# Performance work log

Hardware: AMD Instinct MI355X
Metric: run time of the kernel (lower is better)

## Reference

```python
import jax, jax.numpy as jnp
import numpy as np

N = 100000      # nodes
E = 1600000     # edges
F_IN = 64       # num_features
H = 64          # nhid
G = 512         # num graphs in batch
C = 2           # num_classes
BN_EPS = 1e-5


def setup_inputs() -> dict:
    key = jax.random.key(0)
    ks = jax.random.split(key, 8)
    x = jax.random.normal(ks[0], (N, F_IN), jnp.float32)
    edge_index = jax.random.randint(ks[1], (2, E), 0, N, dtype=jnp.int64)
    batch = jnp.sort(jax.random.randint(ks[2], (N,), 0, G, dtype=jnp.int64))
    s = lambda k, shp, fan: (jax.random.normal(k, shp, jnp.float32) / np.sqrt(fan)).astype(jnp.float32)
    W1 = s(ks[3], (F_IN, H), F_IN); b1 = jnp.zeros((H,), jnp.float32)
    W2 = s(ks[4], (H, H), H);       b2 = jnp.zeros((H,), jnp.float32)
    Wg = s(ks[5], (H, 1), H);       bg = jnp.zeros((1,), jnp.float32)
    bn_gamma = jnp.ones((H,), jnp.float32); bn_beta = jnp.zeros((H,), jnp.float32)
    bn_mean = jnp.zeros((H,), jnp.float32); bn_var = jnp.ones((H,), jnp.float32)
    W_lin = s(ks[6], (H, C), H);    b_lin = jnp.zeros((C,), jnp.float32)
    return dict(x=x, edge_index=edge_index, batch=batch,
                W1=W1, b1=b1, W2=W2, b2=b2, Wg=Wg, bg=bg,
                bn_gamma=bn_gamma, bn_beta=bn_beta, bn_mean=bn_mean, bn_var=bn_var,
                W_lin=W_lin, b_lin=b_lin)


def reference(x, edge_index, batch, W1, b1, W2, b2, Wg, bg,
              bn_gamma, bn_beta, bn_mean, bn_var, W_lin, b_lin):
    src, dst = edge_index[0], edge_index[1]
    # GINConv (eps=0): h_i = MLP(x_i + sum_{j->i} x_j)
    agg = jax.ops.segment_sum(x[src], dst, num_segments=N)       # [N, F_IN]
    h = x + agg
    h = jnp.maximum(h @ W1 + b1, 0.0) @ W2 + b2                  # [N, H]
    h = jnp.maximum(h, 0.0)                                      # outer ReLU
    # Attentional aggregation: segment softmax of gate, weighted segment-sum
    gate = (h @ Wg + bg)[:, 0]                                   # [N]
    gmax = jax.ops.segment_max(gate, batch, num_segments=G)      # [G]
    ex = jnp.exp(gate - gmax[batch])                             # [N]
    denom = jax.ops.segment_sum(ex, batch, num_segments=G)       # [G]
    alpha = ex / denom[batch]                                    # [N]
    pooled = jax.ops.segment_sum(alpha[:, None] * h, batch, num_segments=G)  # [G, H]
    # BatchNorm1d in eval mode (running stats); dropout is identity in eval
    norm = (pooled - bn_mean) / jnp.sqrt(bn_var + BN_EPS) * bn_gamma + bn_beta
    logits = norm @ W_lin + b_lin                                # [G, C]
    return jax.nn.log_softmax(logits, axis=-1)
```

## Files before the change

kernel.cpp:

```cpp
#include <hip/hip_runtime.h>
#include <math.h>
#include <float.h>

#define BN_EPS 1e-5f
#define PBLK   8192
#define NBUCKP 832
#define ACAP   4096
#define STCAP  3072

typedef short s16x8 __attribute__((ext_vector_type(8)));
typedef float f32x4 __attribute__((ext_vector_type(4)));

__device__ __forceinline__ unsigned short f2bf(float f) {
    unsigned u = __float_as_uint(f);
    u += 0x7FFFu + ((u >> 16) & 1u);
    return (unsigned short)(u >> 16);
}
__device__ __forceinline__ float bf2f(unsigned short b) {
    return __uint_as_float(((unsigned)b) << 16);
}
__device__ __forceinline__ int vtb(int row, int byteoff) {
    return row * 128 + (byteoff ^ ((row & 7) << 4));
}

__global__ __launch_bounds__(512) void prep_partition(
    const float* __restrict__ W1, const float* __restrict__ W2,
    unsigned short* __restrict__ w1t, unsigned short* __restrict__ w2t,
    const int* __restrict__ src, const int* __restrict__ dst,
    const int* __restrict__ batch, int* __restrict__ gstart,
    int* __restrict__ bcur0, int* __restrict__ packed2,
    int N, int E, int EB, int G)
{
    __shared__ int hist[NBUCKP], lstart[NBUCKP], goff[NBUCKP], cur[NBUCKP];
    __shared__ int sorted[PBLK];
    __shared__ unsigned short sbkt[PBLK];

    int tid = threadIdx.x;
    int lane = tid & 63;
    int blk = blockIdx.x;

    for (int i = blk * 512 + tid; i < N; i += gridDim.x * 512) {
        int bi = batch[i];
        int bp = (i == 0) ? -1 : batch[i - 1];
        for (int g = bp + 1; g <= bi; ++g) gstart[g] = i;
        if (i == N - 1)
            for (int g = bi + 1; g <= G; ++g) gstart[g] = N;
    }
    if (blk == 0)
        for (int idx = tid; idx < 4096; idx += 512)
            w1t[idx] = f2bf(W1[(idx & 63) * 64 + (idx >> 6)]);
    if (blk == 1)
        for (int idx = tid; idx < 4096; idx += 512)
            w2t[idx] = f2bf(W2[(idx & 63) * 64 + (idx >> 6)]);

    if (blk >= EB) return;

    int e0 = blk * PBLK;
    int cnt = E - e0; if (cnt > PBLK) cnt = PBLK; if (cnt < 0) cnt = 0;

    for (int i = tid; i < NBUCKP; i += 512) hist[i] = 0;
    __syncthreads();
    for (int i = tid; i < cnt; i += 512)
        atomicAdd(&hist[dst[e0 + i] >> 7], 1);
    __syncthreads();
    if (tid < 64) {
        int carry = 0;
        #pragma unroll
        for (int c = 0; c < NBUCKP / 64; ++c) {
            int idx = c * 64 + lane;
            int v = hist[idx];
            int xv = v;
            #pragma unroll
            for (int d = 1; d < 64; d <<= 1) {
                int t = __shfl_up(xv, d); if (lane >= d) xv += t;
            }
            lstart[idx] = xv - v + carry;
            carry += __shfl(xv, 63);
        }
    }
    __syncthreads();
    for (int i = tid; i < NBUCKP; i += 512) {
        cur[i] = lstart[i];
        if (hist[i] > 0) goff[i] = atomicAdd(&bcur0[i], hist[i]);
    }
    __syncthreads();
    for (int i = tid; i < cnt; i += 512) {
        int d = dst[e0 + i];
        int s = src[e0 + i];
        int b = d >> 7;
        int p = atomicAdd(&cur[b], 1);
        sorted[p] = ((d & 127) << 17) | s;
        sbkt[p] = (unsigned short)b;
    }
    __syncthreads();
    for (int i = tid; i < cnt; i += 512) {
        int b = sbkt[i];
        packed2[(size_t)b * ACAP + goff[b] + (i - lstart[b])] = sorted[i];
    }
}

__global__ __launch_bounds__(512, 4) void bucket_fused(
    const float* __restrict__ x,
    const int* __restrict__ packed2, const int* __restrict__ bcur0,
    const unsigned short* __restrict__ w1t, const unsigned short* __restrict__ w2t,
    const float* __restrict__ b1, const float* __restrict__ b2,
    const float* __restrict__ Wg, const float* __restrict__ bg,
    unsigned short* __restrict__ h_out, float* __restrict__ gate_out, int N)
{
    __shared__ char vt_raw[16384];
    __shared__ int stage[STCAP];
    int* hist = (int*)vt_raw;
    int* cur  = hist + 128;
    int* excl = (int*)(vt_raw + 1024);

    int tid = threadIdx.x;
    int lane = tid & 63;
    int wave = tid >> 6;
    int b = blockIdx.x;
    int node0 = b * 128;
    int ecnt = bcur0[b];
    if (ecnt > ACAP) ecnt = ACAP;
    const int* arena = packed2 + (size_t)b * ACAP;

    if (tid < 128) hist[tid] = 0;
    __syncthreads();
    for (int i = tid; i < ecnt; i += 512)
        atomicAdd(&hist[arena[i] >> 17], 1);
    __syncthreads();

    if (tid < 64) {
        int carry = 0;
        #pragma unroll
        for (int c = 0; c < 2; ++c) {
            int idx = c * 64 + lane;
            int v = hist[idx];
            int xv = v;
            #pragma unroll
            for (int d = 1; d < 64; d <<= 1) {
                int t = __shfl_up(xv, d); if (lane >= d) xv += t;
            }
            excl[idx] = xv - v + carry;
            cur[idx]  = xv - v + carry;
            carry += __shfl(xv, 63);
        }
        if (lane == 0) excl[128] = carry;
    }
    __syncthreads();

    for (int i = tid; i < ecnt; i += 512) {
        int v = arena[i];
        int p = atomicAdd(&cur[v >> 17], 1);
        if (p < STCAP) stage[p] = v & 0x1FFFF;
    }
    __syncthreads();

    int rowbase = wave * 16;
    int exv = excl[rowbase + (lane < 17 ? lane : 16)];
    if (exv > STCAP) exv = STCAP;
    __syncthreads();

    for (int m = 0; m < 16; ++m) {
        int ln = rowbase + m;
        int node = node0 + ln;
        if (node < N) {
            int beg  = __builtin_amdgcn_readlane(exv, m);
            int end_ = __builtin_amdgcn_readlane(exv, m + 1);

            float v0 = x[(unsigned)node * 64u + lane];
            float v1 = 0.f, v2 = 0.f, v3 = 0.f, v4 = 0.f, v5 = 0.f, v6 = 0.f, v7 = 0.f;

            for (int base = beg; base < end_; base += 64) {
                int eiv = (base + lane < end_) ? stage[base + lane] : 0;
                int cnt = end_ - base; if (cnt > 64) cnt = 64;
                int j = 0;
                for (; j + 16 <= cnt; j += 16) {
                    int s0  = __builtin_amdgcn_readlane(eiv, j + 0);
                    int s1  = __builtin_amdgcn_readlane(eiv, j + 1);
                    int s2  = __builtin_amdgcn_readlane(eiv, j + 2);
                    int s3  = __builtin_amdgcn_readlane(eiv, j + 3);
                    int s4  = __builtin_amdgcn_readlane(eiv, j + 4);
                    int s5  = __builtin_amdgcn_readlane(eiv, j + 5);
                    int s6  = __builtin_amdgcn_readlane(eiv, j + 6);
                    int s7  = __builtin_amdgcn_readlane(eiv, j + 7);
                    int s8  = __builtin_amdgcn_readlane(eiv, j + 8);
                    int s9  = __builtin_amdgcn_readlane(eiv, j + 9);
                    int s10 = __builtin_amdgcn_readlane(eiv, j + 10);
                    int s11 = __builtin_amdgcn_readlane(eiv, j + 11);
                    int s12 = __builtin_amdgcn_readlane(eiv, j + 12);
                    int s13 = __builtin_amdgcn_readlane(eiv, j + 13);
                    int s14 = __builtin_amdgcn_readlane(eiv, j + 14);
                    int s15 = __builtin_amdgcn_readlane(eiv, j + 15);
                    float t0  = x[(unsigned)s0  * 64u + lane];
                    float t1  = x[(unsigned)s1  * 64u + lane];
                    float t2  = x[(unsigned)s2  * 64u + lane];
                    float t3  = x[(unsigned)s3  * 64u + lane];
                    float t4  = x[(unsigned)s4  * 64u + lane];
                    float t5  = x[(unsigned)s5  * 64u + lane];
                    float t6  = x[(unsigned)s6  * 64u + lane];
                    float t7  = x[(unsigned)s7  * 64u + lane];
                    float t8  = x[(unsigned)s8  * 64u + lane];
                    float t9  = x[(unsigned)s9  * 64u + lane];
                    float t10 = x[(unsigned)s10 * 64u + lane];
                    float t11 = x[(unsigned)s11 * 64u + lane];
                    float t12 = x[(unsigned)s12 * 64u + lane];
                    float t13 = x[(unsigned)s13 * 64u + lane];
                    float t14 = x[(unsigned)s14 * 64u + lane];
                    float t15 = x[(unsigned)s15 * 64u + lane];
                    v0 += t0; v1 += t1; v2 += t2; v3 += t3;
                    v4 += t4; v5 += t5; v6 += t6; v7 += t7;
                    v0 += t8; v1 += t9; v2 += t10; v3 += t11;
                    v4 += t12; v5 += t13; v6 += t14; v7 += t15;
                }
                for (; j + 8 <= cnt; j += 8) {
                    int s0 = __builtin_amdgcn_readlane(eiv, j + 0);
                    int s1 = __builtin_amdgcn_readlane(eiv, j + 1);
                    int s2 = __builtin_amdgcn_readlane(eiv, j + 2);
                    int s3 = __builtin_amdgcn_readlane(eiv, j + 3);
                    int s4 = __builtin_amdgcn_readlane(eiv, j + 4);
                    int s5 = __builtin_amdgcn_readlane(eiv, j + 5);
                    int s6 = __builtin_amdgcn_readlane(eiv, j + 6);
                    int s7 = __builtin_amdgcn_readlane(eiv, j + 7);
                    float t0 = x[(unsigned)s0 * 64u + lane];
                    float t1 = x[(unsigned)s1 * 64u + lane];
                    float t2 = x[(unsigned)s2 * 64u + lane];
                    float t3 = x[(unsigned)s3 * 64u + lane];
                    float t4 = x[(unsigned)s4 * 64u + lane];
                    float t5 = x[(unsigned)s5 * 64u + lane];
                    float t6 = x[(unsigned)s6 * 64u + lane];
                    float t7 = x[(unsigned)s7 * 64u + lane];
                    v0 += t0; v1 += t1; v2 += t2; v3 += t3;
                    v4 += t4; v5 += t5; v6 += t6; v7 += t7;
                }
                for (; j + 4 <= cnt; j += 4) {
                    int s0 = __builtin_amdgcn_readlane(eiv, j + 0);
                    int s1 = __builtin_amdgcn_readlane(eiv, j + 1);
                    int s2 = __builtin_amdgcn_readlane(eiv, j + 2);
                    int s3 = __builtin_amdgcn_readlane(eiv, j + 3);
                    float t0 = x[(unsigned)s0 * 64u + lane];
                    float t1 = x[(unsigned)s1 * 64u + lane];
                    float t2 = x[(unsigned)s2 * 64u + lane];
                    float t3 = x[(unsigned)s3 * 64u + lane];
                    v4 += t0; v5 += t1; v6 += t2; v7 += t3;
                }
                for (; j < cnt; ++j) {
                    int s = __builtin_amdgcn_readlane(eiv, j);
                    v1 += x[(unsigned)s * 64u + lane];
                }
            }
            float v = ((v0 + v1) + (v2 + v3)) + ((v4 + v5) + (v6 + v7));
            *(unsigned short*)(vt_raw + vtb(ln, lane * 2)) = f2bf(v);
        } else {
            *(unsigned short*)(vt_raw + vtb(ln, lane * 2)) = 0;
        }
    }

    {
        int quad = lane >> 4;
        int col  = lane & 15;

        s16x8 a0 = *(const s16x8*)(vt_raw + vtb(rowbase + col, quad * 16));
        s16x8 a1 = *(const s16x8*)(vt_raw + vtb(rowbase + col, 64 + quad * 16));

        float b1v[4], b2v[4], wgv[4];
        #pragma unroll
        for (int nt = 0; nt < 4; ++nt) {
            b1v[nt] = b1[nt * 16 + col];
            b2v[nt] = b2[nt * 16 + col];
            wgv[nt] = Wg[nt * 16 + col];
        }
        float bgv = bg[0];

        f32x4 acc1[4];
        #pragma unroll
        for (int nt = 0; nt < 4; ++nt) {
            int off = (nt * 16 + col) * 64 + quad * 8;
            s16x8 w0 = *(const s16x8*)(w1t + off);
            s16x8 w1 = *(const s16x8*)(w1t + off + 32);
            f32x4 c = {0.f, 0.f, 0.f, 0.f};
            c = __builtin_amdgcn_mfma_f32_16x16x32_bf16(a0, w0, c, 0, 0, 0);
            c = __builtin_amdgcn_mfma_f32_16x16x32_bf16(a1, w1, c, 0, 0, 0);
            acc1[nt] = c;
        }
        #pragma unroll
        for (int nt = 0; nt < 4; ++nt)
            #pragma unroll
            for (int r = 0; r < 4; ++r) {
                float hv = fmaxf(acc1[nt][r] + b1v[nt], 0.f);
                *(unsigned short*)(vt_raw + vtb(rowbase + quad * 4 + r, (nt * 16 + col) * 2)) = f2bf(hv);
            }

        s16x8 g0 = *(const s16x8*)(vt_raw + vtb(rowbase + col, quad * 16));
        s16x8 g1 = *(const s16x8*)(vt_raw + vtb(rowbase + col, 64 + quad * 16));

        f32x4 acc2[4];
        #pragma unroll
        for (int nt = 0; nt < 4; ++nt) {
            int off = (nt * 16 + col) * 64 + quad * 8;
            s16x8 w0 = *(const s16x8*)(w2t + off);
            s16x8 w1 = *(const s16x8*)(w2t + off + 32);
            f32x4 c = {0.f, 0.f, 0.f, 0.f};
            c = __builtin_amdgcn_mfma_f32_16x16x32_bf16(g0, w0, c, 0, 0, 0);
            c = __builtin_amdgcn_mfma_f32_16x16x32_bf16(g1, w1, c, 0, 0, 0);
            acc2[nt] = c;
        }

        int nbase = node0 + rowbase;
        float gp[4] = {0.f, 0.f, 0.f, 0.f};
        #pragma unroll
        for (int nt = 0; nt < 4; ++nt)
            #pragma unroll
            for (int r = 0; r < 4; ++r) {
                float hv = fmaxf(acc2[nt][r] + b2v[nt], 0.f);
                int node = nbase + quad * 4 + r;
                if (node < N)
                    h_out[(size_t)node * 64 + nt * 16 + col] = f2bf(hv);
                gp[r] = fmaf(hv, wgv[nt], gp[r]);
            }
        #pragma unroll
        for (int r = 0; r < 4; ++r) {
            float t = gp[r];
            t += __shfl_xor(t, 1);
            t += __shfl_xor(t, 2);
            t += __shfl_xor(t, 4);
            t += __shfl_xor(t, 8);
            int node = nbase + quad * 4 + r;
            if (col == 0 && node < N) gate_out[node] = t + bgv;
        }
    }
}

__global__ __launch_bounds__(512) void pool_final(
    const unsigned short* __restrict__ h, const float* __restrict__ gate,
    const int* __restrict__ gstart,
    const float* __restrict__ gamma_, const float* __restrict__ beta_,
    const float* __restrict__ mean_, const float* __restrict__ var_,
    const float* __restrict__ Wl, const float* __restrict__ bl,
    float* __restrict__ out)
{
    int g = blockIdx.x;
    int tid = threadIdx.x;

    int start = gstart[g];
    int end   = gstart[g + 1];

    __shared__ float red_m[8], red_s[8];
    __shared__ float pool_s[8 * 64];

    int lane = tid & 63;
    int wave = tid >> 6;

    float m = -FLT_MAX, s = 0.f;
    for (int i = start + tid; i < end; i += 512) {
        float gv = gate[i];
        if (gv > m) { s = s * __expf(m - gv) + 1.f; m = gv; }
        else        { s += __expf(gv - m); }
    }
    #pragma unroll
    for (int off = 32; off; off >>= 1) {
        float mo = __shfl_xor(m, off);
        float so = __shfl_xor(s, off);
        float mn = fmaxf(m, mo);
        s = s * __expf(m - mn) + so * __expf(mo - mn);
        m = mn;
    }
    if (lane == 0) { red_m[wave] = m; red_s[wave] = s; }
    __syncthreads();
    {
        float mn = red_m[0];
        #pragma unroll
        for (int w = 1; w < 8; ++w) mn = fmaxf(mn, red_m[w]);
        float ss = 0.f;
        #pragma unroll
        for (int w = 0; w < 8; ++w) ss += red_s[w] * __expf(red_m[w] - mn);
        m = mn; s = ss;
    }

    float a0 = 0.f, a1 = 0.f, a2 = 0.f, a3 = 0.f;
    int i = start + wave;
    for (; i + 24 < end; i += 32) {
        float e0 = expf(gate[i]      - m);
        float e1 = expf(gate[i + 8]  - m);
        float e2 = expf(gate[i + 16] - m);
        float e3 = expf(gate[i + 24] - m);
        float t0 = bf2f(h[(size_t)(i)      * 64 + lane]);
        float t1 = bf2f(h[(size_t)(i + 8)  * 64 + lane]);
        float t2 = bf2f(h[(size_t)(i + 16) * 64 + lane]);
        float t3 = bf2f(h[(size_t)(i + 24) * 64 + lane]);
        a0 = fmaf(e0, t0, a0);
        a1 = fmaf(e1, t1, a1);
        a2 = fmaf(e2, t2, a2);
        a3 = fmaf(e3, t3, a3);
    }
    for (; i < end; i += 8) {
        float e = expf(gate[i] - m);
        a0 = fmaf(e, bf2f(h[(size_t)i * 64 + lane]), a0);
    }
    pool_s[wave * 64 + lane] = (a0 + a1) + (a2 + a3);
    __syncthreads();

    if (wave == 0) {
        float p = 0.f;
        #pragma unroll
        for (int w = 0; w < 8; ++w) p += pool_s[w * 64 + lane];
        p = (end > start) ? (p / s) : 0.f;
        float nrm = (p - mean_[lane]) / sqrtf(var_[lane] + BN_EPS) * gamma_[lane] + beta_[lane];
        float l0 = nrm * Wl[lane * 2 + 0];
        float l1 = nrm * Wl[lane * 2 + 1];
        #pragma unroll
        for (int off = 32; off; off >>= 1) {
            l0 += __shfl_xor(l0, off);
            l1 += __shfl_xor(l1, off);
        }
        if (lane == 0) {
            l0 += bl[0];
            l1 += bl[1];
            float mx = fmaxf(l0, l1);
            float lse = mx + logf(expf(l0 - mx) + expf(l1 - mx));
            out[g * 2 + 0] = l0 - lse;
            out[g * 2 + 1] = l1 - lse;
        }
    }
}

extern "C" void kernel_launch(void* const* d_in, const int* in_sizes, int n_in,
                              void* d_out, int out_size, void* d_ws, size_t ws_size,
                              hipStream_t stream)
{
    const float* x     = (const float*)d_in[0];
    const int*   eidx  = (const int*)d_in[1];
    const int*   batch = (const int*)d_in[2];
    const float* W1    = (const float*)d_in[3];
    const float* b1    = (const float*)d_in[4];
    const float* W2    = (const float*)d_in[5];
    const float* b2    = (const float*)d_in[6];
    const float* Wg    = (const float*)d_in[7];
    const float* bg    = (const float*)d_in[8];
    const float* bng   = (const float*)d_in[9];
    const float* bnb   = (const float*)d_in[10];
    const float* bnm   = (const float*)d_in[11];
    const float* bnv   = (const float*)d_in[12];
    const float* Wl    = (const float*)d_in[13];
    const float* bl    = (const float*)d_in[14];
    float* out = (float*)d_out;

    int N = in_sizes[0] / 64;
    int E = in_sizes[1] / 2;
    int G = out_size / 2;
    int NBUCK = (N + 127) / 128;
    int EB = (E + PBLK - 1) / PBLK;
    int GRID_A = EB > 2 ? EB : 2;

    char* w = (char*)d_ws;
    int* packed2 = (int*)w;                     w += (size_t)NBUCK * ACAP * 4;
    float* gate  = (float*)w;                   w += ((size_t)N * 4 + 255) / 256 * 256;
    int* bcur0   = (int*)w;                     w += NBUCKP * 4;
    unsigned short* w1t = (unsigned short*)w;   w += 4096 * 2;
    unsigned short* w2t = (unsigned short*)w;   w += 4096 * 2;
    int* gstart  = (int*)w;                     w += ((size_t)(G + 1) * 4 + 255) / 256 * 256;
    unsigned short* hbuf = (unsigned short*)w;

    const int* src = eidx;
    const int* dst = eidx + E;

    hipMemsetAsync(bcur0, 0, NBUCKP * sizeof(int), stream);

    prep_partition<<<GRID_A, 512, 0, stream>>>(W1, W2, w1t, w2t,
                                               src, dst, batch, gstart,
                                               bcur0, packed2,
                                               N, E, EB, G);

    bucket_fused  <<<NBUCK, 512, 0, stream>>>(x, packed2, bcur0, w1t, w2t,
                                              b1, b2, Wg, bg, hbuf, gate, N);

    pool_final    <<<G, 512, 0, stream>>>(hbuf, gate, gstart, bng, bnb, bnm, bnv,
                                          Wl, bl, out);
}
```

Before: 198.5 us.

## Gather neighbor features from a bf16 copy of x with 4-edge-parallel wave layout

Adds a pass in the partition kernel that converts x to bf16 in workspace, and rewrites the neighbor gather to read 8-byte bf16 chunks. Each wave now handles four edges at once, using ds_bpermute to broadcast indices and cross-quarter shuffles to reduce. This halves the bytes moved by the random gather and issues fewer, wider loads. In exchange it adds a full read and write of x, rounds neighbor features to bf16 before summing, enlarges the partition grid, and drops the occupancy hint on the fused kernel.

```diff
diff --git a/kernel.cpp b/kernel.cpp
--- a/kernel.cpp
+++ b/kernel.cpp
@@ -24,6 +24,7 @@
 }
 
 __global__ __launch_bounds__(512) void prep_partition(
+    const float* __restrict__ x, unsigned short* __restrict__ xb,
     const float* __restrict__ W1, const float* __restrict__ W2,
     unsigned short* __restrict__ w1t, unsigned short* __restrict__ w2t,
     const int* __restrict__ src, const int* __restrict__ dst,
@@ -39,6 +40,13 @@
     int lane = tid & 63;
     int blk = blockIdx.x;
 
+    int n4 = N * 16;
+    for (int i = blk * 512 + tid; i < n4; i += gridDim.x * 512) {
+        float4 f = *(const float4*)(x + (size_t)i * 4);
+        ushort4 o;
+        o.x = f2bf(f.x); o.y = f2bf(f.y); o.z = f2bf(f.z); o.w = f2bf(f.w);
+        *(ushort4*)(xb + (size_t)i * 4) = o;
+    }
     for (int i = blk * 512 + tid; i < N; i += gridDim.x * 512) {
         int bi = batch[i];
         int bp = (i == 0) ? -1 : batch[i - 1];
@@ -99,8 +107,8 @@
     }
 }
 
-__global__ __launch_bounds__(512, 4) void bucket_fused(
-    const float* __restrict__ x,
+__global__ __launch_bounds__(512) void bucket_fused(
+    const unsigned short* __restrict__ xb,
     const int* __restrict__ packed2, const int* __restrict__ bcur0,
     const unsigned short* __restrict__ w1t, const unsigned short* __restrict__ w2t,
     const float* __restrict__ b1, const float* __restrict__ b2,
@@ -159,6 +167,11 @@
     if (exv > STCAP) exv = STCAP;
     __syncthreads();
 
+    int q   = lane >> 4;
+    int c   = lane & 15;
+    int qsh = q << 2;
+    unsigned coff = (unsigned)(c * 4);
+
     for (int m = 0; m < 16; ++m) {
         int ln = rowbase + m;
         int node = node0 + ln;
@@ -166,91 +179,65 @@
             int beg  = __builtin_amdgcn_readlane(exv, m);
             int end_ = __builtin_amdgcn_readlane(exv, m + 1);
 
-            float v0 = x[(unsigned)node * 64u + lane];
-            float v1 = 0.f, v2 = 0.f, v3 = 0.f, v4 = 0.f, v5 = 0.f, v6 = 0.f, v7 = 0.f;
+            float a0 = 0.f, a1 = 0.f, a2 = 0.f, a3 = 0.f;
 
             for (int base = beg; base < end_; base += 64) {
                 int eiv = (base + lane < end_) ? stage[base + lane] : 0;
-                int cnt = end_ - base; if (cnt > 64) cnt = 64;
-                int j = 0;
-                for (; j + 16 <= cnt; j += 16) {
-                    int s0  = __builtin_amdgcn_readlane(eiv, j + 0);
-                    int s1  = __builtin_amdgcn_readlane(eiv, j + 1);
-                    int s2  = __builtin_amdgcn_readlane(eiv, j + 2);
-                    int s3  = __builtin_amdgcn_readlane(eiv, j + 3);
-                    int s4  = __builtin_amdgcn_readlane(eiv, j + 4);
-                    int s5  = __builtin_amdgcn_readlane(eiv, j + 5);
-                    int s6  = __builtin_amdgcn_readlane(eiv, j + 6);
-                    int s7  = __builtin_amdgcn_readlane(eiv, j + 7);
-                    int s8  = __builtin_amdgcn_readlane(eiv, j + 8);
-                    int s9  = __builtin_amdgcn_readlane(eiv, j + 9);
-                    int s10 = __builtin_amdgcn_readlane(eiv, j + 10);
-                    int s11 = __builtin_amdgcn_readlane(eiv, j + 11);
-                    int s12 = __builtin_amdgcn_readlane(eiv, j + 12);
-                    int s13 = __builtin_amdgcn_readlane(eiv, j + 13);
-                    int s14 = __builtin_amdgcn_readlane(eiv, j + 14);
-                    int s15 = __builtin_amdgcn_readlane(eiv, j + 15);
-                    float t0  = x[(unsigned)s0  * 64u + lane];
-                    float t1  = x[(unsigned)s1  * 64u + lane];
-                    float t2  = x[(unsigned)s2  * 64u + lane];
-                    float t3  = x[(unsigned)s3  * 64u + lane];
-                    float t4  = x[(unsigned)s4  * 64u + lane];
-                    float t5  = x[(unsigned)s5  * 64u + lane];
-                    float t6  = x[(unsigned)s6  * 64u + lane];
-                    float t7  = x[(unsigned)s7  * 64u + lane];
-                    float t8  = x[(unsigned)s8  * 64u + lane];
-                    float t9  = x[(unsigned)s9  * 64u + lane];
-                    float t10 = x[(unsigned)s10 * 64u + lane];
-                    float t11 = x[(unsigned)s11 * 64u + lane];
-                    float t12 = x[(unsigned)s12 * 64u + lane];
-                    float t13 = x[(unsigned)s13 * 64u + lane];
-                    float t14 = x[(unsigned)s14 * 64u + lane];
-                    float t15 = x[(unsigned)s15 * 64u + lane];
-                    v0 += t0; v1 += t1; v2 += t2; v3 += t3;
-                    v4 += t4; v5 += t5; v6 += t6; v7 += t7;
-                    v0 += t8; v1 += t9; v2 += t10; v3 += t11;
-                    v4 += t12; v5 += t13; v6 += t14; v7 += t15;
+                int deg = end_ - base; if (deg > 64) deg = 64;
+                int kfull = deg >> 2;
+                int k = 0;
+                for (; k + 2 <= kfull; k += 2) {
+                    int sA = __builtin_amdgcn_ds_bpermute((k << 4) + qsh, eiv);
+                    int sB = __builtin_amdgcn_ds_bpermute(((k + 1) << 4) + qsh, eiv);
+                    uint2 dA = *(const uint2*)(xb + (unsigned)sA * 64u + coff);
+                    uint2 dB = *(const uint2*)(xb + (unsigned)sB * 64u + coff);
+                    a0 += __uint_as_float(dA.x << 16);
+                    a1 += __uint_as_float(dA.x & 0xFFFF0000u);
+                    a2 += __uint_as_float(dA.y << 16);
+                    a3 += __uint_as_float(dA.y & 0xFFFF0000u);
+                    a0 += __uint_as_float(dB.x << 16);
+                    a1 += __uint_as_float(dB.x & 0xFFFF0000u);
+                    a2 += __uint_as_float(dB.y << 16);
+                    a3 += __uint_as_float(dB.y & 0xFFFF0000u);
                 }
-                for (; j + 8 <= cnt; j += 8) {
-                    int s0 = __builtin_amdgcn_readlane(eiv, j + 0);
-                    int s1 = __builtin_amdgcn_readlane(eiv, j + 1);
-                    int s2 = __builtin_amdgcn_readlane(eiv, j + 2);
-                    int s3 = __builtin_amdgcn_readlane(eiv, j + 3);
-                    int s4 = __builtin_amdgcn_readlane(eiv, j + 4);
-                    int s5 = __builtin_amdgcn_readlane(eiv, j + 5);
-                    int s6 = __builtin_amdgcn_readlane(eiv, j + 6);
-                    int s7 = __builtin_amdgcn_readlane(eiv, j + 7);
-                    float t0 = x[(unsigned)s0 * 64u + lane];
-                    float t1 = x[(unsigned)s1 * 64u + lane];
-                    float t2 = x[(unsigned)s2 * 64u + lane];
-                    float t3 = x[(unsigned)s3 * 64u + lane];
-                    float t4 = x[(unsigned)s4 * 64u + lane];
-                    float t5 = x[(unsigned)s5 * 64u + lane];
-                    float t6 = x[(unsigned)s6 * 64u + lane];
-                    float t7 = x[(unsigned)s7 * 64u + lane];
-                    v0 += t0; v1 += t1; v2 += t2; v3 += t3;
-                    v4 += t4; v5 += t5; v6 += t6; v7 += t7;
+                for (; k < kfull; ++k) {
+                    int s = __builtin_amdgcn_ds_bpermute((k << 4) + qsh, eiv);
+                    uint2 d = *(const uint2*)(xb + (unsigned)s * 64u + coff);
+                    a0 += __uint_as_float(d.x << 16);
+                    a1 += __uint_as_float(d.x & 0xFFFF0000u);
+                    a2 += __uint_as_float(d.y << 16);
+                    a3 += __uint_as_float(d.y & 0xFFFF0000u);
                 }
-                for (; j + 4 <= cnt; j += 4) {
-                    int s0 = __builtin_amdgcn_readlane(eiv, j + 0);
-                    int s1 = __builtin_amdgcn_readlane(eiv, j + 1);
-                    int s2 = __builtin_amdgcn_readlane(eiv, j + 2);
-                    int s3 = __builtin_amdgcn_readlane(eiv, j + 3);
-                    float t0 = x[(unsigned)s0 * 64u + lane];
-                    float t1 = x[(unsigned)s1 * 64u + lane];
-                    float t2 = x[(unsigned)s2 * 64u + lane];
-                    float t3 = x[(unsigned)s3 * 64u + lane];
-                    v4 += t0; v5 += t1; v6 += t2; v7 += t3;
+                if (deg & 3) {
+                    int e  = (kfull << 2) + q;
+                    int ec = (e < deg) ? e : (deg - 1);
+                    int s  = __builtin_amdgcn_ds_bpermute(ec << 2, eiv);
+                    float msk = (e < deg) ? 1.f : 0.f;
+                    uint2 d = *(const uint2*)(xb + (unsigned)s * 64u + coff);
+                    a0 = fmaf(__uint_as_float(d.x << 16),          msk, a0);
+                    a1 = fmaf(__uint_as_float(d.x & 0xFFFF0000u),  msk, a1);
+                    a2 = fmaf(__uint_as_float(d.y << 16),          msk, a2);
+                    a3 = fmaf(__uint_as_float(d.y & 0xFFFF0000u),  msk, a3);
                 }
-                for (; j < cnt; ++j) {
-                    int s = __builtin_amdgcn_readlane(eiv, j);
-                    v1 += x[(unsigned)s * 64u + lane];
-                }
-            }
-            float v = ((v0 + v1) + (v2 + v3)) + ((v4 + v5) + (v6 + v7));
-            *(unsigned short*)(vt_raw + vtb(ln, lane * 2)) = f2bf(v);
-        } else {
-            *(unsigned short*)(vt_raw + vtb(ln, lane * 2)) = 0;
+            }
+            a0 += __shfl_xor(a0, 16); a1 += __shfl_xor(a1, 16);
+            a2 += __shfl_xor(a2, 16); a3 += __shfl_xor(a3, 16);
+            a0 += __shfl_xor(a0, 32); a1 += __shfl_xor(a1, 32);
+            a2 += __shfl_xor(a2, 32); a3 += __shfl_xor(a3, 32);
+            uint2 sd = *(const uint2*)(xb + (unsigned)node * 64u + coff);
+            a0 += __uint_as_float(sd.x << 16);
+            a1 += __uint_as_float(sd.x & 0xFFFF0000u);
+            a2 += __uint_as_float(sd.y << 16);
+            a3 += __uint_as_float(sd.y & 0xFFFF0000u);
+            if (q == 0) {
+                unsigned lo = (unsigned)f2bf(a0) | ((unsigned)f2bf(a1) << 16);
+                unsigned hi = (unsigned)f2bf(a2) | ((unsigned)f2bf(a3) << 16);
+                uint2 pk = {lo, hi};
+                *(uint2*)(vt_raw + vtb(ln, c * 8)) = pk;
+            }
+        } else if (q == 0) {
+            uint2 z = {0u, 0u};
+            *(uint2*)(vt_raw + vtb(ln, c * 8)) = z;
         }
     }
 
@@ -276,10 +263,10 @@
             int off = (nt * 16 + col) * 64 + quad * 8;
             s16x8 w0 = *(const s16x8*)(w1t + off);
             s16x8 w1 = *(const s16x8*)(w1t + off + 32);
-            f32x4 c = {0.f, 0.f, 0.f, 0.f};
-            c = __builtin_amdgcn_mfma_f32_16x16x32_bf16(a0, w0, c, 0, 0, 0);
-            c = __builtin_amdgcn_mfma_f32_16x16x32_bf16(a1, w1, c, 0, 0, 0);
-            acc1[nt] = c;
+            f32x4 cc = {0.f, 0.f, 0.f, 0.f};
+            cc = __builtin_amdgcn_mfma_f32_16x16x32_bf16(a0, w0, cc, 0, 0, 0);
+            cc = __builtin_amdgcn_mfma_f32_16x16x32_bf16(a1, w1, cc, 0, 0, 0);
+            acc1[nt] = cc;
         }
         #pragma unroll
         for (int nt = 0; nt < 4; ++nt)
@@ -298,10 +285,10 @@
             int off = (nt * 16 + col) * 64 + quad * 8;
             s16x8 w0 = *(const s16x8*)(w2t + off);
             s16x8 w1 = *(const s16x8*)(w2t + off + 32);
-            f32x4 c = {0.f, 0.f, 0.f, 0.f};
-            c = __builtin_amdgcn_mfma_f32_16x16x32_bf16(g0, w0, c, 0, 0, 0);
-            c = __builtin_amdgcn_mfma_f32_16x16x32_bf16(g1, w1, c, 0, 0, 0);
-            acc2[nt] = c;
+            f32x4 cc = {0.f, 0.f, 0.f, 0.f};
+            cc = __builtin_amdgcn_mfma_f32_16x16x32_bf16(g0, w0, cc, 0, 0, 0);
+            cc = __builtin_amdgcn_mfma_f32_16x16x32_bf16(g1, w1, cc, 0, 0, 0);
+            acc2[nt] = cc;
         }
 
         int nbase = node0 + rowbase;
@@ -446,12 +433,14 @@
     int N = in_sizes[0] / 64;
     int E = in_sizes[1] / 2;
     int G = out_size / 2;
+    int NP = ((N + 63) / 64) * 64;
     int NBUCK = (N + 127) / 128;
     int EB = (E + PBLK - 1) / PBLK;
-    int GRID_A = EB > 2 ? EB : 2;
+    int GRID_A = 1024 > EB ? 1024 : EB;
 
     char* w = (char*)d_ws;
     int* packed2 = (int*)w;                     w += (size_t)NBUCK * ACAP * 4;
+    unsigned short* hxb  = (unsigned short*)w;  w += (size_t)NP * 64 * 2;
     float* gate  = (float*)w;                   w += ((size_t)N * 4 + 255) / 256 * 256;
     int* bcur0   = (int*)w;                     w += NBUCKP * 4;
     unsigned short* w1t = (unsigned short*)w;   w += 4096 * 2;
@@ -464,12 +453,12 @@
 
     hipMemsetAsync(bcur0, 0, NBUCKP * sizeof(int), stream);
 
-    prep_partition<<<GRID_A, 512, 0, stream>>>(W1, W2, w1t, w2t,
+    prep_partition<<<GRID_A, 512, 0, stream>>>(x, hxb, W1, W2, w1t, w2t,
                                                src, dst, batch, gstart,
                                                bcur0, packed2,
                                                N, E, EB, G);
 
-    bucket_fused  <<<NBUCK, 512, 0, stream>>>(x, packed2, bcur0, w1t, w2t,
+    bucket_fused  <<<NBUCK, 512, 0, stream>>>(hxb, packed2, bcur0, w1t, w2t,
                                               b1, b2, Wg, bg, hbuf, gate, N);
 
     pool_final    <<<G, 512, 0, stream>>>(hbuf, gate, gstart, bng, bnb, bnm, bnv,
```

Measured after the change: 178.7 us. -10.0%, faster.
